# Kernel tuning notes

Hardware: AMD Instinct MI355X
Metric: run time of the kernel (lower is better)

## Reference

```python
import jax, jax.numpy as jnp
import numpy as np

B, S, D_IN, D_OUT = 4, 2048, 1024, 1024


def setup_inputs() -> dict:
    key = jax.random.key(0)
    kx, kq, kk, kv = jax.random.split(key, 4)
    scale = 1.0 / np.sqrt(D_IN)
    return {
        "x": jax.random.normal(kx, (B, S, D_IN), dtype=jnp.float32),
        "W_q": jax.random.normal(kq, (D_IN, D_OUT), dtype=jnp.float32) * scale,
        "W_k": jax.random.normal(kk, (D_IN, D_OUT), dtype=jnp.float32) * scale,
        "W_v": jax.random.normal(kv, (D_IN, D_OUT), dtype=jnp.float32) * scale,
    }


def reference(x, W_q, W_k, W_v):
    # QKV projections (Linear without bias): [B,S,D_out]
    q = jnp.einsum("bsd,de->bse", x, W_q)
    k = jnp.einsum("bsd,de->bse", x, W_k)
    v = jnp.einsum("bsd,de->bse", x, W_v)

    # Raw scores [B,S,S], causal mask (strict upper triangle -> -inf),
    # then scale by sqrt(d_k) and softmax, matching the torch order of ops.
    scores = jnp.einsum("bqd,bkd->bqk", q, k)
    seq = scores.shape[-1]
    causal = jnp.triu(jnp.ones((seq, seq), dtype=bool), k=1)
    scores = jnp.where(causal[None, :, :], -jnp.inf, scores)
    attn = jax.nn.softmax(scores / jnp.sqrt(jnp.asarray(q.shape[-1], scores.dtype)), axis=-1)
    # dropout p=0.0 -> identity (eval semantics)
    return jnp.einsum("bqk,bkd->bqd", attn, v)
```

## Files before the change

kernel.cpp:

```cpp
#include <hip/hip_runtime.h>

typedef unsigned short u16;
typedef __bf16 bf16x8 __attribute__((ext_vector_type(8)));
typedef float f32x4 __attribute__((ext_vector_type(4)));

__device__ __forceinline__ u16 f2bf(float f) {
    union { float f; unsigned int u; } v; v.f = f;
    unsigned int u = v.u;
    return (u16)((u + 0x7FFFu + ((u >> 16) & 1u)) >> 16);
}

__device__ __forceinline__ void load_lds16(const void* g, void* l) {
    __builtin_amdgcn_global_load_lds(
        (const __attribute__((address_space(1))) unsigned int*)g,
        (__attribute__((address_space(3))) unsigned int*)l,
        16, 0, 0);
}

__global__ void __launch_bounds__(256) prep_kernel(
    const float4* __restrict__ X, u16* __restrict__ xb,
    const float* __restrict__ Wq, const float* __restrict__ Wk,
    const float* __restrict__ Wv,
    u16* __restrict__ Oq, u16* __restrict__ Ok, u16* __restrict__ Ov) {
    __shared__ float tile[32][33];
    const int bid = blockIdx.x, tid = threadIdx.x;
    if (bid < 8192) {
        int idx = bid * 256 + tid;
        float4 v = X[idx];
        ushort4 o;
        o.x = f2bf(v.x); o.y = f2bf(v.y); o.z = f2bf(v.z); o.w = f2bf(v.w);
        *(ushort4*)(xb + (size_t)idx * 4) = o;
    } else {
        int id = bid - 8192;
        int zz = id >> 10;
        const float* W = (zz == 0) ? Wq : (zz == 1) ? Wk : Wv;
        u16* O = (zz == 0) ? Oq : (zz == 1) ? Ok : Ov;
        int n0 = (id & 31) * 32, k0 = ((id >> 5) & 31) * 32;
        int tx = tid & 31, ty = tid >> 5;
        #pragma unroll
        for (int j = 0; j < 32; j += 8)
            tile[ty + j][tx] = W[(size_t)(k0 + ty + j) * 1024 + n0 + tx];
        __syncthreads();
        #pragma unroll
        for (int j = 0; j < 32; j += 8)
            O[(size_t)(n0 + ty + j) * 1024 + k0 + tx] = f2bf(tile[tx][ty + j]);
    }
}

template <int MODE>
__global__ void __launch_bounds__(256) gemm_nt(
    const u16* __restrict__ xb, const u16* __restrict__ WqT,
    const u16* __restrict__ WkT, const u16* __restrict__ WvT,
    u16* __restrict__ Q, u16* __restrict__ Kb,
    u16* __restrict__ Vt, u16* __restrict__ S,
    float* __restrict__ out) {

    int mtile, ntile, z;
    const u16 *A, *B;
    int vsub = 0;

    if (MODE == 0) {
        int L = blockIdx.x;
        int c = L & 7, t = (L >> 3) & 7, hi = L >> 6;
        int p = hi * 8 + c;
        z = p >> 6; mtile = p & 63; ntile = t;
        A = xb;
        B = z ? WkT : WqT;
    } else if (MODE == 1) {
        if (blockIdx.x < 512) {
            vsub = 1;
            int id = blockIdx.x;
            int c = id & 7, t = (id >> 3) & 7, hi = id >> 6;
            mtile = hi * 8 + c; ntile = t; z = 0;
            A = xb; B = WvT;
        } else {
            int id2 = blockIdx.x - 512;
            z = id2 / 192;
            int r = id2 - z * 192;
            int c = r & 7, g = r >> 3;
            if (g <= c)            { mtile = c;     ntile = g; }
            else if (g < 2*c + 10) { mtile = c + 8; ntile = g - (c + 1); }
            else return;
            A = Q  + (size_t)z * (2048 * 1024);
            B = Kb + (size_t)z * (2048 * 1024);
        }
    } else {
        int L = blockIdx.x;
        int c = L & 7, j = (L >> 3) & 7, h = L >> 6;
        int P = h * 8 + c;
        z = P & 3; mtile = 15 - (P >> 2); ntile = j;
        A = S  + (size_t)z * (2048 * 2048);
        B = Vt + (size_t)z * (1024 * 2048);
    }

    const int LDA = (MODE == 3) ? 2048 : 1024;
    const int kiters = (MODE == 3) ? (mtile + 1) * 2 : 16;

    __shared__ __align__(16) u16 As[2][128 * 32];
    __shared__ __align__(16) u16 Bs[2][128 * 32];

    const int tid = threadIdx.x;
    const int lane = tid & 63;
    const int wave = tid >> 6;
    const int wr = wave >> 1, wc = wave & 1;

    const int r0 = tid >> 2;
    const int kb = (((tid & 3) ^ ((r0 >> 1) & 3))) * 16;

    const char* gA0 = (const char*)(A + (size_t)(mtile * 128 + r0) * LDA) + kb;
    const char* gA1 = gA0 + (size_t)64 * LDA * 2;
    const char* gB0 = (const char*)(B + (size_t)(ntile * 128 + r0) * LDA) + kb;
    const char* gB1 = gB0 + (size_t)64 * LDA * 2;

    char* lA = (char*)(&As[0][0]) + tid * 16;
    char* lB = (char*)(&Bs[0][0]) + tid * 16;

    f32x4 acc[4][4] = {};
    f32x4 acc_rs[4] = {};

    bf16x8 vones;
    #pragma unroll
    for (int i = 0; i < 8; ++i) vones[i] = (__bf16)1.0f;

    const int quad = lane >> 4;
    const int l16 = lane & 15;
    const int ch = quad ^ ((l16 >> 1) & 3);
    const int aoff = (wr * 64 + l16) * 32 + ch * 8;
    const int boff = (wc * 64 + l16) * 32 + ch * 8;

    for (int kt = 0; kt < kiters; ++kt) {
        load_lds16(gA0,      lA);
        load_lds16(gA1,      lA + 4096);
        load_lds16(gA0 + 64, lA + 8192);
        load_lds16(gA1 + 64, lA + 12288);
        load_lds16(gB0,      lB);
        load_lds16(gB1,      lB + 4096);
        load_lds16(gB0 + 64, lB + 8192);
        load_lds16(gB1 + 64, lB + 12288);
        gA0 += 128; gA1 += 128; gB0 += 128; gB1 += 128;
        __syncthreads();

        #pragma unroll
        for (int h2 = 0; h2 < 2; ++h2) {
            const u16* ap = &As[h2][aoff];
            const u16* bp = &Bs[h2][boff];
            bf16x8 af[4], bfv[4];
            #pragma unroll
            for (int r = 0; r < 4; ++r) af[r] = *(const bf16x8*)(ap + r * 512);
            #pragma unroll
            for (int c = 0; c < 4; ++c) bfv[c] = *(const bf16x8*)(bp + c * 512);
            if (MODE == 3) {
                #pragma unroll
                for (int r = 0; r < 4; ++r)
                    acc_rs[r] = __builtin_amdgcn_mfma_f32_16x16x32_bf16(
                        af[r], vones, acc_rs[r], 0, 0, 0);
            }
            #pragma unroll
            for (int r = 0; r < 4; ++r)
                #pragma unroll
                for (int c = 0; c < 4; ++c)
                    acc[r][c] = __builtin_amdgcn_mfma_f32_16x16x32_bf16(
                        af[r], bfv[c], acc[r][c], 0, 0, 0);
        }
        __syncthreads();
    }

    const int grow0 = mtile * 128 + wr * 64 + quad * 4;
    const int gcol0 = ntile * 128 + wc * 64 + l16;

    if (MODE == 0) {
        u16* C = z ? Kb : Q;
        #pragma unroll
        for (int r = 0; r < 4; ++r)
            #pragma unroll
            for (int c = 0; c < 4; ++c)
                #pragma unroll
                for (int i = 0; i < 4; ++i)
                    C[(size_t)(grow0 + r * 16 + i) * 1024 + gcol0 + c * 16] =
                        f2bf(acc[r][c][i]);
    } else if (MODE == 1) {
        if (vsub) {
            #pragma unroll
            for (int r = 0; r < 4; ++r) {
                int m0 = grow0 + r * 16;
                int b = m0 >> 11, s0 = m0 & 2047;
                #pragma unroll
                for (int c = 0; c < 4; ++c) {
                    int d = gcol0 + c * 16;
                    ushort4 o;
                    o.x = f2bf(acc[r][c][0]); o.y = f2bf(acc[r][c][1]);
                    o.z = f2bf(acc[r][c][2]); o.w = f2bf(acc[r][c][3]);
                    *(ushort4*)(Vt + (size_t)b * (1024 * 2048) + (size_t)d * 2048 + s0) = o;
                }
            }
        } else {
            u16* C = S + (size_t)z * (2048 * 2048);
            const bool diag = (ntile == mtile);
            #pragma unroll
            for (int r = 0; r < 4; ++r)
                #pragma unroll
                for (int c = 0; c < 4; ++c)
                    #pragma unroll
                    for (int i = 0; i < 4; ++i) {
                        int grow = grow0 + r * 16 + i;
                        int gcol = gcol0 + c * 16;
                        float e = 0.f;
                        if (!diag || gcol <= grow)
                            e = __expf(acc[r][c][i] * 0.03125f - 12.0f);
                        C[(size_t)grow * 2048 + gcol] = f2bf(e);
                    }
        }
    } else {
        float* C = out + (size_t)z * (2048 * 1024);
        #pragma unroll
        for (int r = 0; r < 4; ++r)
            #pragma unroll
            for (int i = 0; i < 4; ++i) {
                int grow = grow0 + r * 16 + i;
                float inv = 1.0f / acc_rs[r][i];
                #pragma unroll
                for (int c = 0; c < 4; ++c)
                    C[(size_t)grow * 1024 + gcol0 + c * 16] = acc[r][c][i] * inv;
            }
    }
}

extern "C" void kernel_launch(void* const* d_in, const int* in_sizes, int n_in,
                              void* d_out, int out_size, void* d_ws, size_t ws_size,
                              hipStream_t stream) {
    const float* x  = (const float*)d_in[0];
    const float* Wq = (const float*)d_in[1];
    const float* Wk = (const float*)d_in[2];
    const float* Wv = (const float*)d_in[3];
    float* out = (float*)d_out;
    char* ws = (char*)d_ws;
    const size_t Mi = 1u << 20;

    u16* xb  = (u16*)(ws);
    u16* WqT = (u16*)(ws + 16 * Mi);
    u16* WkT = (u16*)(ws + 18 * Mi);
    u16* WvT = (u16*)(ws + 20 * Mi);
    u16* Q   = (u16*)(ws + 22 * Mi);
    u16* Kb  = (u16*)(ws + 38 * Mi);
    u16* Vt  = (u16*)(ws + 54 * Mi);
    u16* S   = (u16*)(ws + 70 * Mi);

    prep_kernel<<<11264, 256, 0, stream>>>(
        (const float4*)x, xb, Wq, Wk, Wv, WqT, WkT, WvT);

    gemm_nt<0><<<1024, 256, 0, stream>>>(xb, WqT, WkT, WvT, Q, Kb, Vt, S, out);

    gemm_nt<1><<<1280, 256, 0, stream>>>(xb, WqT, WkT, WvT, Q, Kb, Vt, S, out);

    gemm_nt<3><<<512, 256, 0, stream>>>(xb, WqT, WkT, WvT, Q, Kb, Vt, S, out);
}
```

Measured before the change: 231.1 us.

## Compute softmax row sums in score epilogue via atomics instead of ones-MFMA

The softmax denominator is now built in the score GEMM epilogue. Each tile's exponentials are summed per row, reduced across lanes with shuffles, and atomically added to a rowsum buffer that the prep kernel zeroes. This removes the extra ones-vector MFMAs from the inner loop of the P·V GEMM. The P·V block-to-tile mapping is also simplified. The cost is shuffles and global float atomics in the epilogue. Row sums now come from unrounded fp32 exponentials rather than the bf16 values actually stored in S.

```diff
diff --git a/kernel.cpp b/kernel.cpp
--- a/kernel.cpp
+++ b/kernel.cpp
@@ -21,7 +21,8 @@
     const float4* __restrict__ X, u16* __restrict__ xb,
     const float* __restrict__ Wq, const float* __restrict__ Wk,
     const float* __restrict__ Wv,
-    u16* __restrict__ Oq, u16* __restrict__ Ok, u16* __restrict__ Ov) {
+    u16* __restrict__ Oq, u16* __restrict__ Ok, u16* __restrict__ Ov,
+    float* __restrict__ rowsum) {
     __shared__ float tile[32][33];
     const int bid = blockIdx.x, tid = threadIdx.x;
     if (bid < 8192) {
@@ -30,7 +31,7 @@
         ushort4 o;
         o.x = f2bf(v.x); o.y = f2bf(v.y); o.z = f2bf(v.z); o.w = f2bf(v.w);
         *(ushort4*)(xb + (size_t)idx * 4) = o;
-    } else {
+    } else if (bid < 11264) {
         int id = bid - 8192;
         int zz = id >> 10;
         const float* W = (zz == 0) ? Wq : (zz == 1) ? Wk : Wv;
@@ -44,6 +45,8 @@
         #pragma unroll
         for (int j = 0; j < 32; j += 8)
             O[(size_t)(n0 + ty + j) * 1024 + k0 + tx] = f2bf(tile[tx][ty + j]);
+    } else {
+        rowsum[(bid - 11264) * 256 + tid] = 0.f;
     }
 }
 
@@ -53,7 +56,7 @@
     const u16* __restrict__ WkT, const u16* __restrict__ WvT,
     u16* __restrict__ Q, u16* __restrict__ Kb,
     u16* __restrict__ Vt, u16* __restrict__ S,
-    float* __restrict__ out) {
+    float* __restrict__ rowsum, float* __restrict__ out) {
 
     int mtile, ntile, z;
     const u16 *A, *B;
@@ -86,9 +89,9 @@
         }
     } else {
         int L = blockIdx.x;
-        int c = L & 7, j = (L >> 3) & 7, h = L >> 6;
-        int P = h * 8 + c;
-        z = P & 3; mtile = 15 - (P >> 2); ntile = j;
+        ntile = L & 7;
+        int j = L >> 3;
+        z = j & 3; mtile = 15 - (j >> 2);
         A = S  + (size_t)z * (2048 * 2048);
         B = Vt + (size_t)z * (1024 * 2048);
     }
@@ -116,11 +119,6 @@
     char* lB = (char*)(&Bs[0][0]) + tid * 16;
 
     f32x4 acc[4][4] = {};
-    f32x4 acc_rs[4] = {};
-
-    bf16x8 vones;
-    #pragma unroll
-    for (int i = 0; i < 8; ++i) vones[i] = (__bf16)1.0f;
 
     const int quad = lane >> 4;
     const int l16 = lane & 15;
@@ -149,12 +147,6 @@
             for (int r = 0; r < 4; ++r) af[r] = *(const bf16x8*)(ap + r * 512);
             #pragma unroll
             for (int c = 0; c < 4; ++c) bfv[c] = *(const bf16x8*)(bp + c * 512);
-            if (MODE == 3) {
-                #pragma unroll
-                for (int r = 0; r < 4; ++r)
-                    acc_rs[r] = __builtin_amdgcn_mfma_f32_16x16x32_bf16(
-                        af[r], vones, acc_rs[r], 0, 0, 0);
-            }
             #pragma unroll
             for (int r = 0; r < 4; ++r)
                 #pragma unroll
@@ -195,7 +187,13 @@
             }
         } else {
             u16* C = S + (size_t)z * (2048 * 2048);
+            float* rs = rowsum + z * 2048;
             const bool diag = (ntile == mtile);
+            float rsum[4][4];
+            #pragma unroll
+            for (int r = 0; r < 4; ++r)
+                #pragma unroll
+                for (int i = 0; i < 4; ++i) rsum[r][i] = 0.f;
             #pragma unroll
             for (int r = 0; r < 4; ++r)
                 #pragma unroll
@@ -208,16 +206,30 @@
                         if (!diag || gcol <= grow)
                             e = __expf(acc[r][c][i] * 0.03125f - 12.0f);
                         C[(size_t)grow * 2048 + gcol] = f2bf(e);
+                        rsum[r][i] += e;
                     }
+            #pragma unroll
+            for (int r = 0; r < 4; ++r)
+                #pragma unroll
+                for (int i = 0; i < 4; ++i) {
+                    float s = rsum[r][i];
+                    s += __shfl_xor(s, 1, 64);
+                    s += __shfl_xor(s, 2, 64);
+                    s += __shfl_xor(s, 4, 64);
+                    s += __shfl_xor(s, 8, 64);
+                    if (l16 == 0)
+                        atomicAdd(&rs[grow0 + r * 16 + i], s);
+                }
         }
     } else {
+        const float* rs = rowsum + z * 2048;
         float* C = out + (size_t)z * (2048 * 1024);
         #pragma unroll
         for (int r = 0; r < 4; ++r)
             #pragma unroll
             for (int i = 0; i < 4; ++i) {
                 int grow = grow0 + r * 16 + i;
-                float inv = 1.0f / acc_rs[r][i];
+                float inv = 1.0f / rs[grow];
                 #pragma unroll
                 for (int c = 0; c < 4; ++c)
                     C[(size_t)grow * 1024 + gcol0 + c * 16] = acc[r][c][i] * inv;
@@ -244,13 +256,14 @@
     u16* Kb  = (u16*)(ws + 38 * Mi);
     u16* Vt  = (u16*)(ws + 54 * Mi);
     u16* S   = (u16*)(ws + 70 * Mi);
-
-    prep_kernel<<<11264, 256, 0, stream>>>(
-        (const float4*)x, xb, Wq, Wk, Wv, WqT, WkT, WvT);
-
-    gemm_nt<0><<<1024, 256, 0, stream>>>(xb, WqT, WkT, WvT, Q, Kb, Vt, S, out);
-
-    gemm_nt<1><<<1280, 256, 0, stream>>>(xb, WqT, WkT, WvT, Q, Kb, Vt, S, out);
-
-    gemm_nt<3><<<512, 256, 0, stream>>>(xb, WqT, WkT, WvT, Q, Kb, Vt, S, out);
-}
+    float* rowsum = (float*)(ws + 102 * Mi);
+
+    prep_kernel<<<11296, 256, 0, stream>>>(
+        (const float4*)x, xb, Wq, Wk, Wv, WqT, WkT, WvT, rowsum);
+
+    gemm_nt<0><<<1024, 256, 0, stream>>>(xb, WqT, WkT, WvT, Q, Kb, Vt, S, rowsum, out);
+
+    gemm_nt<1><<<1280, 256, 0, stream>>>(xb, WqT, WkT, WvT, Q, Kb, Vt, S, rowsum, out);
+
+    gemm_nt<3><<<512, 256, 0, stream>>>(xb, WqT, WkT, WvT, Q, Kb, Vt, S, rowsum, out);
+}
```

Result: slower. 236.3 us (+2.2%).
